# Kernel optimization log

Measured on AMD Instinct MI355X. Metric: run time of the kernel, lower is better.

The kernel has to match this reference:

```python
import jax, jax.numpy as jnp
import numpy as np

NUM_CLASSES = 10
PGD_NUMS = 10
ALPHA = 0.15
# Hardcoded in the original module: sign vector for 10 classes
SIGN_VEC = jnp.array([-1.0] * 4 + [1.0] * 6, dtype=jnp.float32)


def setup_inputs() -> dict:
    key = jax.random.key(0)
    k1, k2, k3 = jax.random.split(key, 3)
    B = 1048576
    logit = jax.random.normal(k1, (B, NUM_CLASSES), dtype=jnp.float32)
    y = jax.random.randint(k2, (B,), 0, NUM_CLASSES, dtype=jnp.int32)
    label_freq = jax.random.randint(k3, (NUM_CLASSES,), 0, PGD_NUMS, dtype=jnp.int32)
    return {"logit": logit, "y": y, "label_freq": label_freq}


def _compute_adv(logit, y):
    # softmax over classes, then per-class mean of softmax rows (one-hot^T @ p)
    p = jax.nn.softmax(logit, axis=-1)  # [B, C]
    sum_class_logit = jax.ops.segment_sum(p, y, num_segments=NUM_CLASSES)  # [C, C]
    counts = jax.ops.segment_sum(jnp.ones(y.shape[0], dtype=logit.dtype), y,
                                 num_segments=NUM_CLASSES)  # [C]
    counts = jnp.where(counts == 0, jnp.asarray(100.0, logit.dtype), counts)
    mean_class_logit = sum_class_logit / counts[:, None]  # [C, C]
    grad = mean_class_logit - jnp.eye(NUM_CLASSES, dtype=logit.dtype)
    # Faithful to torch: norm over dim=0 (columns), then reshape(-1,1) divides row i
    col_norm = jnp.linalg.norm(grad, axis=0)  # [C]
    grad = grad / col_norm[:, None]
    grad = ALPHA * grad * SIGN_VEC[:, None].astype(logit.dtype)
    return grad[y]  # index_select along dim 0 -> [B, C]


def reference(logit, y, label_freq):
    logit_copy = logit

    def step(l, _):
        l_new = l + _compute_adv(l, y)
        return l_new, l_new

    _, logit_steps = jax.lax.scan(step, logit, None, length=PGD_NUMS)  # [P, B, C]

    # Original: logit_news = sum_i logit_steps[label_freq[i]] * (y == i)
    # Since class masks are disjoint, this is a per-sample gather of step label_freq[y[n]].
    steps_per_sample = label_freq[y]  # [B]
    B = logit.shape[0]
    logit_news = logit_steps[steps_per_sample, jnp.arange(B)]  # [B, C]

    # mean cross-entropy
    log_p = jax.nn.log_softmax(logit_news, axis=-1)
    loss_adv = -jnp.mean(jnp.take_along_axis(log_p, y[:, None].astype(jnp.int32), axis=1))
    return loss_adv, logit_news, logit_copy
```

## Files before the change

kernel.cpp:

```cpp
#include <hip/hip_runtime.h>

#define PGD   10
#define ALPHA 0.15f
#define NTAB  32
#define SPT   8
#define NTHR  256

#define WS_COUNTS 0
#define WS_STAB   320
#define WS_DGLOB  32320
#define WS_ZERO_N 33320

__global__ void k_init(float* __restrict__ ws, float* __restrict__ out) {
    int i = blockIdx.x * blockDim.x + threadIdx.x;
    if (i == 0) out[0] = 0.f;
    int gs = gridDim.x * blockDim.x;
    for (int k = i; k < WS_ZERO_N; k += gs) ws[k] = 0.f;
}

__global__ __launch_bounds__(NTHR, 2) void k_step(
    const float* __restrict__ logit, const int* __restrict__ y,
    float* __restrict__ ws, int B, int t )
{
    __shared__ float tab[100][NTAB];
    __shared__ float ctab[10][NTAB];
    __shared__ float sh_D[100];
    __shared__ float shT[100];
    __shared__ float shCnt[10];
    __shared__ float shCn[10];

    const int tid = threadIdx.x;
    const int gth = gridDim.x * NTHR;
    const int base = blockIdx.x * NTHR + tid;

    float* counts_tab = ws + WS_COUNTS;
    float* S_tab      = ws + WS_STAB;
    float* D_glob     = ws + WS_DGLOB;

    float xv[SPT][10];
    int   yc[SPT];
    #pragma unroll
    for (int k = 0; k < SPT; ++k) {
        int idx = base + k * gth;
        if (idx < B) {
            yc[k] = y[idx];
            const float2* rp = reinterpret_cast<const float2*>(logit + (size_t)idx * 10);
            #pragma unroll
            for (int q = 0; q < 5; ++q) {
                float2 v = rp[q];
                xv[k][2 * q] = v.x; xv[k][2 * q + 1] = v.y;
            }
        } else {
            yc[k] = -1;
            #pragma unroll
            for (int j = 0; j < 10; ++j) xv[k][j] = 0.f;
        }
    }

    for (int i = tid; i < 100 * NTAB; i += NTHR) (&tab[0][0])[i] = 0.f;
    if (t == 1) for (int i = tid; i < 10 * NTAB; i += NTHR) (&ctab[0][0])[i] = 0.f;

    if (t >= 2) {
        const float* Sg = S_tab + (size_t)(t - 2) * (NTAB * 100);
        if (tid < 10) {
            float s = 0.f;
            #pragma unroll
            for (int k = 0; k < NTAB; ++k) s += counts_tab[k * 10 + tid];
            shCnt[tid] = (s == 0.f) ? 100.f : s;
        }
        if (tid < 100) {
            float s = 0.f;
            #pragma unroll
            for (int k = 0; k < NTAB; ++k) s += Sg[k * 100 + tid];
            shT[tid] = s;
        }
        __syncthreads();
        if (tid < 100) {
            int c = tid / 10, j = tid - c * 10;
            shT[tid] = shT[tid] / shCnt[c] - ((c == j) ? 1.f : 0.f);
        }
        __syncthreads();
        if (tid < 10) {
            float s = 0.f;
            for (int cc = 0; cc < 10; ++cc) { float g = shT[cc * 10 + tid]; s += g * g; }
            shCn[tid] = sqrtf(s);
        }
        __syncthreads();
        if (tid < 100) {
            int c = tid / 10;
            float sign = (c < 4) ? -1.f : 1.f;
            float g = shT[tid] / shCn[c] * (ALPHA * sign);
            sh_D[tid] = ((t >= 3) ? D_glob[(size_t)(t - 3) * 100 + tid] : 0.f) + g;
        }
        __syncthreads();
        if (blockIdx.x == 0 && tid < 100) D_glob[(size_t)(t - 2) * 100 + tid] = sh_D[tid];
    }
    __syncthreads();

    const int lane31 = tid & 31;
    #pragma unroll
    for (int k = 0; k < SPT; ++k) {
        int c = yc[k];
        if (c < 0) continue;
        float tv[10];
        #pragma unroll
        for (int j = 0; j < 10; ++j) tv[j] = xv[k][j];
        if (t >= 2) {
            #pragma unroll
            for (int j = 0; j < 10; ++j) tv[j] += sh_D[c * 10 + j];
        }
        float m = tv[0];
        #pragma unroll
        for (int j = 1; j < 10; ++j) m = fmaxf(m, tv[j]);
        float s = 0.f;
        #pragma unroll
        for (int j = 0; j < 10; ++j) { tv[j] = __expf(tv[j] - m); s += tv[j]; }
        float r = 1.f / s;
        #pragma unroll
        for (int j = 0; j < 10; ++j) unsafeAtomicAdd(&tab[c * 10 + j][lane31], tv[j] * r);
        if (t == 1) unsafeAtomicAdd(&ctab[c][lane31], 1.f);
    }
    __syncthreads();

    const int tb = blockIdx.x & (NTAB - 1);
    if (tid < 100) {
        float s = 0.f;
        #pragma unroll
        for (int k = 0; k < NTAB; ++k) s += tab[tid][(tid + k) & (NTAB - 1)];
        unsafeAtomicAdd(&S_tab[(size_t)(t - 1) * (NTAB * 100) + (size_t)tb * 100 + tid], s);
    }
    if (t == 1 && tid < 10) {
        float s = 0.f;
        #pragma unroll
        for (int k = 0; k < NTAB; ++k) s += ctab[tid][(tid + k) & (NTAB - 1)];
        unsafeAtomicAdd(&counts_tab[tb * 10 + tid], s);
    }
}

__global__ __launch_bounds__(NTHR, 2) void k_final(
    const float* __restrict__ logit, const int* __restrict__ y,
    const int* __restrict__ label_freq,
    float* __restrict__ out, float* __restrict__ ws, int B)
{
    __shared__ float Dall[PGD][100];
    __shared__ float shT[100];
    __shared__ float shCnt[10];
    __shared__ float shCn[10];
    __shared__ int   lf[10];
    __shared__ float wsum[4];

    const int tid = threadIdx.x;
    const int gth = gridDim.x * NTHR;
    const int base = blockIdx.x * NTHR + tid;

    float* counts_tab = ws + WS_COUNTS;
    float* S_tab      = ws + WS_STAB;
    float* D_glob     = ws + WS_DGLOB;

    float xv[SPT][10];
    int   yc[SPT];
    #pragma unroll
    for (int k = 0; k < SPT; ++k) {
        int idx = base + k * gth;
        if (idx < B) {
            yc[k] = y[idx];
            const float2* rp = reinterpret_cast<const float2*>(logit + (size_t)idx * 10);
            #pragma unroll
            for (int q = 0; q < 5; ++q) {
                float2 v = rp[q];
                xv[k][2 * q] = v.x; xv[k][2 * q + 1] = v.y;
            }
        } else {
            yc[k] = -1;
            #pragma unroll
            for (int j = 0; j < 10; ++j) xv[k][j] = 0.f;
        }
    }

    {
        const float* Sg = S_tab + (size_t)9 * (NTAB * 100);
        if (tid < 10) {
            float s = 0.f;
            #pragma unroll
            for (int k = 0; k < NTAB; ++k) s += counts_tab[k * 10 + tid];
            shCnt[tid] = (s == 0.f) ? 100.f : s;
        }
        if (tid < 100) {
            float s = 0.f;
            #pragma unroll
            for (int k = 0; k < NTAB; ++k) s += Sg[k * 100 + tid];
            shT[tid] = s;
        }
        __syncthreads();
        if (tid < 100) {
            int c = tid / 10, j = tid - c * 10;
            shT[tid] = shT[tid] / shCnt[c] - ((c == j) ? 1.f : 0.f);
        }
        __syncthreads();
        if (tid < 10) {
            float s = 0.f;
            for (int cc = 0; cc < 10; ++cc) { float g = shT[cc * 10 + tid]; s += g * g; }
            shCn[tid] = sqrtf(s);
        }
        __syncthreads();
        if (tid < 100) {
            int c = tid / 10;
            float sign = (c < 4) ? -1.f : 1.f;
            float g = shT[tid] / shCn[c] * (ALPHA * sign);
            Dall[9][tid] = D_glob[8 * 100 + tid] + g;
        }
        for (int i = tid; i < 900; i += NTHR) Dall[i / 100][i % 100] = D_glob[i];
        if (tid < 10) lf[tid] = label_freq[tid];
        __syncthreads();
    }

    float* news_out = out + 1;
    float* copy_out = out + 1 + (size_t)B * 10;
    float acc = 0.f;
    #pragma unroll
    for (int k = 0; k < SPT; ++k) {
        int idx = base + k * gth;
        if (idx >= B) continue;
        int c = yc[k];
        int sel = lf[c];
        float nv[10];
        #pragma unroll
        for (int j = 0; j < 10; ++j) nv[j] = xv[k][j] + Dall[sel][c * 10 + j];
        float2* np = reinterpret_cast<float2*>(news_out + (size_t)idx * 10);
        float2* cp = reinterpret_cast<float2*>(copy_out + (size_t)idx * 10);
        #pragma unroll
        for (int q = 0; q < 5; ++q) {
            np[q] = make_float2(nv[2 * q], nv[2 * q + 1]);
            cp[q] = make_float2(xv[k][2 * q], xv[k][2 * q + 1]);
        }
        float m = nv[0];
        #pragma unroll
        for (int j = 1; j < 10; ++j) m = fmaxf(m, nv[j]);
        float s = 0.f;
        #pragma unroll
        for (int j = 0; j < 10; ++j) s += __expf(nv[j] - m);
        acc += __logf(s) + m - nv[c];
    }
    #pragma unroll
    for (int off = 32; off > 0; off >>= 1) acc += __shfl_down(acc, off);
    if ((tid & 63) == 0) wsum[tid >> 6] = acc;
    __syncthreads();
    if (tid == 0)
        unsafeAtomicAdd(out, (wsum[0] + wsum[1] + wsum[2] + wsum[3]) / (float)B);
}

extern "C" void kernel_launch(void* const* d_in, const int* in_sizes, int n_in,
                              void* d_out, int out_size, void* d_ws, size_t ws_size,
                              hipStream_t stream) {
    const float* logit = (const float*)d_in[0];
    const int*   yy    = (const int*)d_in[1];
    const int*   lf    = (const int*)d_in[2];
    float* out = (float*)d_out;
    float* ws  = (float*)d_ws;
    int B = in_sizes[0] / 10;

    int blocks = (B + NTHR * SPT - 1) / (NTHR * SPT);

    hipLaunchKernelGGL(k_init, dim3(64), dim3(NTHR), 0, stream, ws, out);
    for (int t = 1; t <= PGD; ++t)
        hipLaunchKernelGGL(k_step, dim3(blocks), dim3(NTHR), 0, stream,
                           logit, yy, ws, B, t);
    hipLaunchKernelGGL(k_final, dim3(blocks), dim3(NTHR), 0, stream,
                       logit, yy, lf, out, ws, B);
}
```

Before: 672.2 us.

## Replace shared-memory atomic tables with per-thread register accumulators and wave shuffles

k_step now keeps a 100-entry class-by-class softmax accumulator plus 10 counts in registers per thread. These are reduced with wavefront xor-shuffles into a small shared table, replacing the per-lane LDS atomic tables. Logits are now loaded after the D-table setup instead of prefetched into registers, and samples per thread drop from 8 to 4, which doubles the grid; k_final gets its own smaller per-thread sample count. The 100-register accumulator with predicated per-class updates costs heavy register use and lowers occupancy. Every step now also pays 110 full-wave shuffle reductions per block.

```diff
diff --git a/kernel.cpp b/kernel.cpp
--- a/kernel.cpp
+++ b/kernel.cpp
@@ -3,8 +3,10 @@
 #define PGD   10
 #define ALPHA 0.15f
 #define NTAB  32
-#define SPT   8
 #define NTHR  256
+#define SPT   4
+#define FTHR  256
+#define FSPT  4
 
 #define WS_COUNTS 0
 #define WS_STAB   320
@@ -18,16 +20,15 @@
     for (int k = i; k < WS_ZERO_N; k += gs) ws[k] = 0.f;
 }
 
-__global__ __launch_bounds__(NTHR, 2) void k_step(
+__global__ __launch_bounds__(NTHR) void k_step(
     const float* __restrict__ logit, const int* __restrict__ y,
     float* __restrict__ ws, int B, int t )
 {
-    __shared__ float tab[100][NTAB];
-    __shared__ float ctab[10][NTAB];
     __shared__ float sh_D[100];
     __shared__ float shT[100];
     __shared__ float shCnt[10];
     __shared__ float shCn[10];
+    __shared__ float wtab[110][5];
 
     const int tid = threadIdx.x;
     const int gth = gridDim.x * NTHR;
@@ -36,29 +37,6 @@
     float* counts_tab = ws + WS_COUNTS;
     float* S_tab      = ws + WS_STAB;
     float* D_glob     = ws + WS_DGLOB;
-
-    float xv[SPT][10];
-    int   yc[SPT];
-    #pragma unroll
-    for (int k = 0; k < SPT; ++k) {
-        int idx = base + k * gth;
-        if (idx < B) {
-            yc[k] = y[idx];
-            const float2* rp = reinterpret_cast<const float2*>(logit + (size_t)idx * 10);
-            #pragma unroll
-            for (int q = 0; q < 5; ++q) {
-                float2 v = rp[q];
-                xv[k][2 * q] = v.x; xv[k][2 * q + 1] = v.y;
-            }
-        } else {
-            yc[k] = -1;
-            #pragma unroll
-            for (int j = 0; j < 10; ++j) xv[k][j] = 0.f;
-        }
-    }
-
-    for (int i = tid; i < 100 * NTAB; i += NTHR) (&tab[0][0])[i] = 0.f;
-    if (t == 1) for (int i = tid; i < 10 * NTAB; i += NTHR) (&ctab[0][0])[i] = 0.f;
 
     if (t >= 2) {
         const float* Sg = S_tab + (size_t)(t - 2) * (NTAB * 100);
@@ -97,14 +75,25 @@
     }
     __syncthreads();
 
-    const int lane31 = tid & 31;
+    float racc[100];
+    float rcnt[10];
+    #pragma unroll
+    for (int i = 0; i < 100; ++i) racc[i] = 0.f;
+    #pragma unroll
+    for (int i = 0; i < 10; ++i) rcnt[i] = 0.f;
+
     #pragma unroll
     for (int k = 0; k < SPT; ++k) {
-        int c = yc[k];
-        if (c < 0) continue;
+        int idx = base + k * gth;
+        if (idx >= B) break;
+        int c = y[idx];
+        const float2* rp = reinterpret_cast<const float2*>(logit + (size_t)idx * 10);
         float tv[10];
         #pragma unroll
-        for (int j = 0; j < 10; ++j) tv[j] = xv[k][j];
+        for (int q = 0; q < 5; ++q) {
+            float2 v = rp[q];
+            tv[2 * q] = v.x; tv[2 * q + 1] = v.y;
+        }
         if (t >= 2) {
             #pragma unroll
             for (int j = 0; j < 10; ++j) tv[j] += sh_D[c * 10 + j];
@@ -117,27 +106,57 @@
         for (int j = 0; j < 10; ++j) { tv[j] = __expf(tv[j] - m); s += tv[j]; }
         float r = 1.f / s;
         #pragma unroll
-        for (int j = 0; j < 10; ++j) unsafeAtomicAdd(&tab[c * 10 + j][lane31], tv[j] * r);
-        if (t == 1) unsafeAtomicAdd(&ctab[c][lane31], 1.f);
+        for (int j = 0; j < 10; ++j) tv[j] *= r;
+        #pragma unroll
+        for (int cc = 0; cc < 10; ++cc) {
+            if (c == cc) {
+                #pragma unroll
+                for (int j = 0; j < 10; ++j) racc[cc * 10 + j] += tv[j];
+                rcnt[cc] += 1.f;
+            }
+        }
+    }
+
+    const int wave = tid >> 6;
+    const bool lane0 = (tid & 63) == 0;
+    #pragma unroll
+    for (int r0 = 0; r0 < 100; ++r0) {
+        float v = racc[r0];
+        v += __shfl_xor(v, 1);
+        v += __shfl_xor(v, 2);
+        v += __shfl_xor(v, 4);
+        v += __shfl_xor(v, 8);
+        v += __shfl_xor(v, 16);
+        v += __shfl_xor(v, 32);
+        if (lane0) wtab[r0][wave] = v;
+    }
+    if (t == 1) {
+        #pragma unroll
+        for (int r0 = 0; r0 < 10; ++r0) {
+            float v = rcnt[r0];
+            v += __shfl_xor(v, 1);
+            v += __shfl_xor(v, 2);
+            v += __shfl_xor(v, 4);
+            v += __shfl_xor(v, 8);
+            v += __shfl_xor(v, 16);
+            v += __shfl_xor(v, 32);
+            if (lane0) wtab[100 + r0][wave] = v;
+        }
     }
     __syncthreads();
 
     const int tb = blockIdx.x & (NTAB - 1);
     if (tid < 100) {
-        float s = 0.f;
-        #pragma unroll
-        for (int k = 0; k < NTAB; ++k) s += tab[tid][(tid + k) & (NTAB - 1)];
+        float s = wtab[tid][0] + wtab[tid][1] + wtab[tid][2] + wtab[tid][3];
         unsafeAtomicAdd(&S_tab[(size_t)(t - 1) * (NTAB * 100) + (size_t)tb * 100 + tid], s);
     }
     if (t == 1 && tid < 10) {
-        float s = 0.f;
-        #pragma unroll
-        for (int k = 0; k < NTAB; ++k) s += ctab[tid][(tid + k) & (NTAB - 1)];
+        float s = wtab[100 + tid][0] + wtab[100 + tid][1] + wtab[100 + tid][2] + wtab[100 + tid][3];
         unsafeAtomicAdd(&counts_tab[tb * 10 + tid], s);
     }
 }
 
-__global__ __launch_bounds__(NTHR, 2) void k_final(
+__global__ __launch_bounds__(FTHR, 2) void k_final(
     const float* __restrict__ logit, const int* __restrict__ y,
     const int* __restrict__ label_freq,
     float* __restrict__ out, float* __restrict__ ws, int B)
@@ -150,17 +169,17 @@
     __shared__ float wsum[4];
 
     const int tid = threadIdx.x;
-    const int gth = gridDim.x * NTHR;
-    const int base = blockIdx.x * NTHR + tid;
+    const int gth = gridDim.x * FTHR;
+    const int base = blockIdx.x * FTHR + tid;
 
     float* counts_tab = ws + WS_COUNTS;
     float* S_tab      = ws + WS_STAB;
     float* D_glob     = ws + WS_DGLOB;
 
-    float xv[SPT][10];
-    int   yc[SPT];
-    #pragma unroll
-    for (int k = 0; k < SPT; ++k) {
+    float xv[FSPT][10];
+    int   yc[FSPT];
+    #pragma unroll
+    for (int k = 0; k < FSPT; ++k) {
         int idx = base + k * gth;
         if (idx < B) {
             yc[k] = y[idx];
@@ -209,7 +228,7 @@
             float g = shT[tid] / shCn[c] * (ALPHA * sign);
             Dall[9][tid] = D_glob[8 * 100 + tid] + g;
         }
-        for (int i = tid; i < 900; i += NTHR) Dall[i / 100][i % 100] = D_glob[i];
+        for (int i = tid; i < 900; i += FTHR) Dall[i / 100][i % 100] = D_glob[i];
         if (tid < 10) lf[tid] = label_freq[tid];
         __syncthreads();
     }
@@ -218,7 +237,7 @@
     float* copy_out = out + 1 + (size_t)B * 10;
     float acc = 0.f;
     #pragma unroll
-    for (int k = 0; k < SPT; ++k) {
+    for (int k = 0; k < FSPT; ++k) {
         int idx = base + k * gth;
         if (idx >= B) continue;
         int c = yc[k];
@@ -259,12 +278,13 @@
     float* ws  = (float*)d_ws;
     int B = in_sizes[0] / 10;
 
-    int blocks = (B + NTHR * SPT - 1) / (NTHR * SPT);
-
-    hipLaunchKernelGGL(k_init, dim3(64), dim3(NTHR), 0, stream, ws, out);
+    int blocks  = (B + NTHR * SPT - 1) / (NTHR * SPT);
+    int fblocks = (B + FTHR * FSPT - 1) / (FTHR * FSPT);
+
+    hipLaunchKernelGGL(k_init, dim3(64), dim3(256), 0, stream, ws, out);
     for (int t = 1; t <= PGD; ++t)
         hipLaunchKernelGGL(k_step, dim3(blocks), dim3(NTHR), 0, stream,
                            logit, yy, ws, B, t);
-    hipLaunchKernelGGL(k_final, dim3(blocks), dim3(NTHR), 0, stream,
+    hipLaunchKernelGGL(k_final, dim3(fblocks), dim3(FTHR), 0, stream,
                        logit, yy, lf, out, ws, B);
 }
```

Result: faster. 566.6 us (-15.7%).

## Use contiguous 4-sample float4 loads and smaller per-wave LDS reduction tables

Applied to the files above, without the earlier changes.

Each thread now handles four consecutive samples and loads them with ten float4 loads plus one int4 label load, replacing strided float2 loads. The 100x32 lane-striped LDS accumulation table becomes an 8x100 table indexed by wave and lane parity, which shrinks LDS use and the final reduction. The data load now happens after the D computation rather than before it, and SPT halves, so the grid doubles. Per-thread accesses are contiguous but warp-level coalescing is strided by 160 bytes, and heavier contention on LDS atomics is a risk.

```diff
diff --git a/kernel.cpp b/kernel.cpp
--- a/kernel.cpp
+++ b/kernel.cpp
@@ -3,8 +3,10 @@
 #define PGD   10
 #define ALPHA 0.15f
 #define NTAB  32
-#define SPT   8
 #define NTHR  256
+#define SPT   4
+#define FTHR  256
+#define FSPT  4
 
 #define WS_COUNTS 0
 #define WS_STAB   320
@@ -18,47 +20,55 @@
     for (int k = i; k < WS_ZERO_N; k += gs) ws[k] = 0.f;
 }
 
-__global__ __launch_bounds__(NTHR, 2) void k_step(
+__device__ __forceinline__ void load4(const float* __restrict__ logit,
+                                      const int* __restrict__ y,
+                                      int s0, int B, float a[40], int yc[4]) {
+    if (s0 + 4 <= B) {
+        const float4* rp = reinterpret_cast<const float4*>(logit + (size_t)s0 * 10);
+        float4 q[10];
+        #pragma unroll
+        for (int i = 0; i < 10; ++i) q[i] = rp[i];
+        int4 yv = *reinterpret_cast<const int4*>(y + s0);
+        #pragma unroll
+        for (int i = 0; i < 10; ++i) {
+            a[4 * i + 0] = q[i].x; a[4 * i + 1] = q[i].y;
+            a[4 * i + 2] = q[i].z; a[4 * i + 3] = q[i].w;
+        }
+        yc[0] = yv.x; yc[1] = yv.y; yc[2] = yv.z; yc[3] = yv.w;
+    } else {
+        #pragma unroll
+        for (int k = 0; k < 4; ++k) {
+            int idx = s0 + k;
+            if (idx < B) {
+                yc[k] = y[idx];
+                for (int j = 0; j < 10; ++j) a[k * 10 + j] = logit[(size_t)idx * 10 + j];
+            } else {
+                yc[k] = -1;
+                for (int j = 0; j < 10; ++j) a[k * 10 + j] = 0.f;
+            }
+        }
+    }
+}
+
+__global__ __launch_bounds__(NTHR) void k_step(
     const float* __restrict__ logit, const int* __restrict__ y,
     float* __restrict__ ws, int B, int t )
 {
-    __shared__ float tab[100][NTAB];
-    __shared__ float ctab[10][NTAB];
     __shared__ float sh_D[100];
     __shared__ float shT[100];
     __shared__ float shCnt[10];
     __shared__ float shCn[10];
+    __shared__ float wtab[8][100];
+    __shared__ float ctab[8][10];
 
     const int tid = threadIdx.x;
-    const int gth = gridDim.x * NTHR;
-    const int base = blockIdx.x * NTHR + tid;
 
     float* counts_tab = ws + WS_COUNTS;
     float* S_tab      = ws + WS_STAB;
     float* D_glob     = ws + WS_DGLOB;
 
-    float xv[SPT][10];
-    int   yc[SPT];
-    #pragma unroll
-    for (int k = 0; k < SPT; ++k) {
-        int idx = base + k * gth;
-        if (idx < B) {
-            yc[k] = y[idx];
-            const float2* rp = reinterpret_cast<const float2*>(logit + (size_t)idx * 10);
-            #pragma unroll
-            for (int q = 0; q < 5; ++q) {
-                float2 v = rp[q];
-                xv[k][2 * q] = v.x; xv[k][2 * q + 1] = v.y;
-            }
-        } else {
-            yc[k] = -1;
-            #pragma unroll
-            for (int j = 0; j < 10; ++j) xv[k][j] = 0.f;
-        }
-    }
-
-    for (int i = tid; i < 100 * NTAB; i += NTHR) (&tab[0][0])[i] = 0.f;
-    if (t == 1) for (int i = tid; i < 10 * NTAB; i += NTHR) (&ctab[0][0])[i] = 0.f;
+    for (int i = tid; i < 800; i += NTHR) (&wtab[0][0])[i] = 0.f;
+    if (t == 1) for (int i = tid; i < 80; i += NTHR) (&ctab[0][0])[i] = 0.f;
 
     if (t >= 2) {
         const float* Sg = S_tab + (size_t)(t - 2) * (NTAB * 100);
@@ -97,14 +107,19 @@
     }
     __syncthreads();
 
-    const int lane31 = tid & 31;
+    const int s0 = (blockIdx.x * NTHR + tid) * SPT;
+    float a[40];
+    int   yc[4];
+    load4(logit, y, s0, B, a, yc);
+
+    const int sub = ((tid >> 6) << 1) | (tid & 1);
     #pragma unroll
     for (int k = 0; k < SPT; ++k) {
         int c = yc[k];
         if (c < 0) continue;
         float tv[10];
         #pragma unroll
-        for (int j = 0; j < 10; ++j) tv[j] = xv[k][j];
+        for (int j = 0; j < 10; ++j) tv[j] = a[k * 10 + j];
         if (t >= 2) {
             #pragma unroll
             for (int j = 0; j < 10; ++j) tv[j] += sh_D[c * 10 + j];
@@ -117,8 +132,8 @@
         for (int j = 0; j < 10; ++j) { tv[j] = __expf(tv[j] - m); s += tv[j]; }
         float r = 1.f / s;
         #pragma unroll
-        for (int j = 0; j < 10; ++j) unsafeAtomicAdd(&tab[c * 10 + j][lane31], tv[j] * r);
-        if (t == 1) unsafeAtomicAdd(&ctab[c][lane31], 1.f);
+        for (int j = 0; j < 10; ++j) unsafeAtomicAdd(&wtab[sub][c * 10 + j], tv[j] * r);
+        if (t == 1) unsafeAtomicAdd(&ctab[sub][c], 1.f);
     }
     __syncthreads();
 
@@ -126,18 +141,18 @@
     if (tid < 100) {
         float s = 0.f;
         #pragma unroll
-        for (int k = 0; k < NTAB; ++k) s += tab[tid][(tid + k) & (NTAB - 1)];
+        for (int w = 0; w < 8; ++w) s += wtab[w][tid];
         unsafeAtomicAdd(&S_tab[(size_t)(t - 1) * (NTAB * 100) + (size_t)tb * 100 + tid], s);
     }
     if (t == 1 && tid < 10) {
         float s = 0.f;
         #pragma unroll
-        for (int k = 0; k < NTAB; ++k) s += ctab[tid][(tid + k) & (NTAB - 1)];
+        for (int w = 0; w < 8; ++w) s += ctab[w][tid];
         unsafeAtomicAdd(&counts_tab[tb * 10 + tid], s);
     }
 }
 
-__global__ __launch_bounds__(NTHR, 2) void k_final(
+__global__ __launch_bounds__(FTHR) void k_final(
     const float* __restrict__ logit, const int* __restrict__ y,
     const int* __restrict__ label_freq,
     float* __restrict__ out, float* __restrict__ ws, int B)
@@ -150,32 +165,10 @@
     __shared__ float wsum[4];
 
     const int tid = threadIdx.x;
-    const int gth = gridDim.x * NTHR;
-    const int base = blockIdx.x * NTHR + tid;
 
     float* counts_tab = ws + WS_COUNTS;
     float* S_tab      = ws + WS_STAB;
     float* D_glob     = ws + WS_DGLOB;
-
-    float xv[SPT][10];
-    int   yc[SPT];
-    #pragma unroll
-    for (int k = 0; k < SPT; ++k) {
-        int idx = base + k * gth;
-        if (idx < B) {
-            yc[k] = y[idx];
-            const float2* rp = reinterpret_cast<const float2*>(logit + (size_t)idx * 10);
-            #pragma unroll
-            for (int q = 0; q < 5; ++q) {
-                float2 v = rp[q];
-                xv[k][2 * q] = v.x; xv[k][2 * q + 1] = v.y;
-            }
-        } else {
-            yc[k] = -1;
-            #pragma unroll
-            for (int j = 0; j < 10; ++j) xv[k][j] = 0.f;
-        }
-    }
 
     {
         const float* Sg = S_tab + (size_t)9 * (NTAB * 100);
@@ -209,29 +202,34 @@
             float g = shT[tid] / shCn[c] * (ALPHA * sign);
             Dall[9][tid] = D_glob[8 * 100 + tid] + g;
         }
-        for (int i = tid; i < 900; i += NTHR) Dall[i / 100][i % 100] = D_glob[i];
+        for (int i = tid; i < 900; i += FTHR) Dall[i / 100][i % 100] = D_glob[i];
         if (tid < 10) lf[tid] = label_freq[tid];
         __syncthreads();
     }
+
+    const int s0 = (blockIdx.x * FTHR + tid) * FSPT;
+    float a[40];
+    int   yc[4];
+    load4(logit, y, s0, B, a, yc);
 
     float* news_out = out + 1;
     float* copy_out = out + 1 + (size_t)B * 10;
     float acc = 0.f;
     #pragma unroll
-    for (int k = 0; k < SPT; ++k) {
-        int idx = base + k * gth;
-        if (idx >= B) continue;
+    for (int k = 0; k < FSPT; ++k) {
+        int idx = s0 + k;
+        if (idx >= B || yc[k] < 0) continue;
         int c = yc[k];
         int sel = lf[c];
         float nv[10];
         #pragma unroll
-        for (int j = 0; j < 10; ++j) nv[j] = xv[k][j] + Dall[sel][c * 10 + j];
+        for (int j = 0; j < 10; ++j) nv[j] = a[k * 10 + j] + Dall[sel][c * 10 + j];
         float2* np = reinterpret_cast<float2*>(news_out + (size_t)idx * 10);
         float2* cp = reinterpret_cast<float2*>(copy_out + (size_t)idx * 10);
         #pragma unroll
         for (int q = 0; q < 5; ++q) {
             np[q] = make_float2(nv[2 * q], nv[2 * q + 1]);
-            cp[q] = make_float2(xv[k][2 * q], xv[k][2 * q + 1]);
+            cp[q] = make_float2(a[k * 10 + 2 * q], a[k * 10 + 2 * q + 1]);
         }
         float m = nv[0];
         #pragma unroll
@@ -259,12 +257,13 @@
     float* ws  = (float*)d_ws;
     int B = in_sizes[0] / 10;
 
-    int blocks = (B + NTHR * SPT - 1) / (NTHR * SPT);
-
-    hipLaunchKernelGGL(k_init, dim3(64), dim3(NTHR), 0, stream, ws, out);
+    int blocks  = (B + NTHR * SPT - 1) / (NTHR * SPT);
+    int fblocks = (B + FTHR * FSPT - 1) / (FTHR * FSPT);
+
+    hipLaunchKernelGGL(k_init, dim3(64), dim3(256), 0, stream, ws, out);
     for (int t = 1; t <= PGD; ++t)
         hipLaunchKernelGGL(k_step, dim3(blocks), dim3(NTHR), 0, stream,
                            logit, yy, ws, B, t);
-    hipLaunchKernelGGL(k_final, dim3(blocks), dim3(NTHR), 0, stream,
+    hipLaunchKernelGGL(k_final, dim3(fblocks), dim3(FTHR), 0, stream,
                        logit, yy, lf, out, ws, B);
 }
```

New measurement: 670.6 us. About the same (-0.2%).
